# Kernel tuning notes

Measured on AMD Instinct MI355X. Metric: run time of the kernel, lower is better.

## Reference

```python
import jax, jax.numpy as jnp
import numpy as np
from jax import lax

B, C, H, W, K = 8, 128, 64, 64, 7
PAD = K // 2
TIMESTEPS = 8
BN_EPS = 1e-3


def _conv(x, w, pad):
    # x: [N,C,H,W], w: [O,I,kh,kw]
    return lax.conv_general_dilated(
        x, w, window_strides=(1, 1),
        padding=[(pad, pad), (pad, pad)],
        dimension_numbers=('NCHW', 'OIHW', 'NCHW'))


def _bn(x, g, b):
    # BatchNorm2d, track_running_stats=False -> always batch stats (biased var)
    m = jnp.mean(x, axis=(0, 2, 3), keepdims=True)
    v = jnp.var(x, axis=(0, 2, 3), keepdims=True)
    return (x - m) * lax.rsqrt(v + BN_EPS) * g[None, :, None, None] + b[None, :, None, None]


def _cb(b):
    return b[None, :, None, None]


def setup_inputs() -> dict:
    key = jax.random.key(0)
    ks = jax.random.split(key, 16)
    n = lambda k, sh, s=0.1: s * jax.random.normal(k, sh, dtype=jnp.float32)
    i_w_b = jax.random.uniform(ks[12], (C,), dtype=jnp.float32, minval=1.0, maxval=TIMESTEPS - 1.0)
    return {
        'input_': jax.random.normal(ks[0], (B, C, H, W), dtype=jnp.float32),
        'inhibition': jax.random.normal(ks[1], (B, C, H, W), dtype=jnp.float32),
        'excitation': jax.random.normal(ks[2], (B, C, H, W), dtype=jnp.float32),
        'a_w_w': n(ks[3], (1, C, K, K)), 'a_w_b': jnp.ones((1,), jnp.float32),
        'a_u_w': n(ks[4], (1, C, K, K)), 'a_u_b': jnp.ones((1,), jnp.float32),
        'i_w_w': n(ks[5], (C, C, 1, 1)), 'i_w_b': i_w_b,
        'i_u_w': n(ks[6], (C, C, 1, 1)), 'i_u_b': n(ks[7], (C,)),
        'e_w_w': n(ks[8], (C, C, 1, 1)), 'e_w_b': -i_w_b,
        'e_u_w': n(ks[9], (C, C, 1, 1)), 'e_u_b': n(ks[10], (C,)),
        'w_inh': n(ks[11], (C, C, K, K), 0.02),
        'w_exc': n(ks[13], (C, C, K, K), 0.02),
        'alpha': 0.1 * jnp.ones((C, 1, 1), jnp.float32),
        'gamma': jnp.ones((C, 1, 1), jnp.float32),
        'kappa': 0.5 * jnp.ones((C, 1, 1), jnp.float32),
        'w_param': 0.5 * jnp.ones((C, 1, 1), jnp.float32),
        'mu': jnp.ones((C, 1, 1), jnp.float32),
        'bn0_g': 0.1 * jnp.ones((C,), jnp.float32), 'bn0_b': jnp.zeros((C,), jnp.float32),
        'bn1_g': 0.1 * jnp.ones((C,), jnp.float32), 'bn1_b': jnp.zeros((C,), jnp.float32),
    }


def reference(input_, inhibition, excitation,
              a_w_w, a_w_b, a_u_w, a_u_b,
              i_w_w, i_w_b, i_u_w, i_u_b,
              e_w_w, e_w_b, e_u_w, e_u_b,
              w_inh, w_exc, alpha, gamma, kappa, w_param, mu,
              bn0_g, bn0_b, bn1_g, bn1_b):
    att_gate = jax.nn.sigmoid(_conv(input_, a_w_w, PAD) + _cb(a_w_b)
                              + _conv(excitation, a_u_w, PAD) + _cb(a_u_b))
    inh_intx = _bn(_conv(excitation * att_gate, w_inh, PAD), bn0_g, bn0_b)
    gated_inhibition = inhibition * att_gate
    gated_input = input_ * att_gate
    inhibition_hat = jnp.tanh(gated_input - jnp.tanh(inh_intx * (alpha * gated_inhibition + mu)))
    inh_gate = jax.nn.sigmoid(_conv(input_, i_w_w, 0) + _cb(i_w_b)
                              + _conv(inhibition, i_u_w, 0) + _cb(i_u_b))
    inhibition = (1.0 - inh_gate) * inhibition + inh_gate * inhibition_hat
    exc_gate = jax.nn.sigmoid(_conv(inhibition, e_w_w, 0) + _cb(e_w_b)
                              + _conv(excitation, e_u_w, 0) + _cb(e_u_b))
    exc_intx = _bn(_conv(inhibition, w_exc, PAD), bn1_g, bn1_b)
    excitation_hat = jnp.tanh(kappa * inhibition + gamma * exc_intx + w_param * inhibition * exc_intx)
    excitation = (1.0 - exc_gate) * excitation + exc_gate * excitation_hat
    return (inhibition, excitation)
```

## Files before the change

### kernel.cpp

```cpp
#include <hip/hip_runtime.h>
#include <cstddef>

typedef _Float16 f16;
typedef _Float16 f16x8 __attribute__((ext_vector_type(8)));
typedef float f32x16 __attribute__((ext_vector_type(16)));

#define Bc   8
#define Cc   128
#define Hc   64
#define Wc   64
#define HWc  4096
#define PADc 3
#define TAPS 49

#define PY 8
#define PX 16
#define WY 14
#define WX 22
#define NPOS (WY*WX)
#define AROW 256
#define ALDS_BYTES (NPOS*AROW)

__global__ __launch_bounds__(256) void prep_kernel(
    const float* __restrict__ w1, const float* __restrict__ w2,
    f16* __restrict__ wt1, f16* __restrict__ wt2, float* __restrict__ att)
{
    int idx = blockIdx.x*256 + threadIdx.x;
    const int NW = TAPS*Cc*Cc;
    if (idx < NW) {
        int tap = idx / (Cc*Cc);
        int rem = idx - tap*(Cc*Cc);
        int co = rem >> 7, ci = rem & 127;
        size_t src = (size_t)(co*Cc + ci)*TAPS + tap;
        wt1[idx] = (f16)w1[src];
        wt2[idx] = (f16)w2[src];
    }
    if (idx < Bc*HWc) att[idx] = 0.f;
}

__global__ __launch_bounds__(128) void att_partial(
    const float* __restrict__ input_, const float* __restrict__ exc,
    const float* __restrict__ aw, const float* __restrict__ au,
    float* __restrict__ att)
{
    __shared__ float wsa[32*49];
    __shared__ float wsb[32*49];
    __shared__ float ti[WY*WX];
    __shared__ float te[WY*WX];
    const int tid = threadIdx.x;
    const int tile = blockIdx.x;
    const int cch  = blockIdx.y*32;
    const int b    = blockIdx.z;
    for (int i = tid; i < 32*49; i += 128) { wsa[i] = aw[cch*49 + i]; wsb[i] = au[cch*49 + i]; }
    const int y0 = (tile >> 2)*8, x0 = (tile & 3)*16;
    const int tx = tid & 15, ty = tid >> 4;
    const float* ib = input_ + (size_t)b*Cc*HWc;
    const float* eb = exc    + (size_t)b*Cc*HWc;
    float acc = 0.f;
    for (int ci = 0; ci < 32; ++ci) {
        __syncthreads();
        for (int i = tid; i < WY*WX; i += 128) {
            int iy = i / WX, ix = i - iy*WX;
            int gy = y0 + iy - PADc, gx = x0 + ix - PADc;
            float v0 = 0.f, v1 = 0.f;
            if (gy >= 0 && gy < Hc && gx >= 0 && gx < Wc) {
                size_t o = (size_t)(cch+ci)*HWc + gy*Wc + gx;
                v0 = ib[o]; v1 = eb[o];
            }
            ti[i] = v0; te[i] = v1;
        }
        __syncthreads();
        const float* wa = &wsa[ci*49];
        const float* wb = &wsb[ci*49];
        #pragma unroll
        for (int kh = 0; kh < 7; ++kh) {
            #pragma unroll
            for (int kw = 0; kw < 7; ++kw) {
                const int k = kh*7+kw;
                acc += ti[(ty+kh)*WX + tx+kw] * wa[k];
                acc += te[(ty+kh)*WX + tx+kw] * wb[k];
            }
        }
    }
    atomicAdd(&att[(size_t)b*HWc + (size_t)(y0+ty)*Wc + (x0+tx)], acc);
}

__global__ __launch_bounds__(256) void att_final(
    float* __restrict__ att, const float* __restrict__ awb, const float* __restrict__ aub)
{
    int i = blockIdx.x*256 + threadIdx.x;
    float z = att[i] + awb[0] + aub[0];
    att[i] = 1.f/(1.f+expf(-z));
}

__global__ __launch_bounds__(256) void conv7_mfma(
    const float* __restrict__ x, const float* __restrict__ att,
    const f16* __restrict__ wt, float* __restrict__ out)
{
    __shared__ unsigned char smem[ALDS_BYTES];
    const int tid = threadIdx.x;
    const int x0 = blockIdx.x * PX;
    const int y0 = blockIdx.y * PY;
    const int b  = blockIdx.z;
    const float* xb = x + (size_t)b*Cc*HWc;

    for (int idx = tid; idx < NPOS*16; idx += 256) {
        int slot = idx / NPOS;
        int pos  = idx - slot*NPOS;
        int r = pos / WX, xw = pos - r*WX;
        int gy = y0 + r - PADc, gx = x0 + xw - PADc;
        bool inb = (gy >= 0 && gy < Hc && gx >= 0 && gx < Wc);
        float g = 1.f;
        if (att) g = inb ? att[(size_t)b*HWc + gy*Wc + gx] : 0.f;
        unsigned int pk[4];
        #pragma unroll
        for (int jj = 0; jj < 4; ++jj) {
            float v0 = 0.f, v1 = 0.f;
            if (inb) {
                size_t o = (size_t)(slot*8 + jj*2)*HWc + (size_t)gy*Wc + gx;
                v0 = xb[o]; v1 = xb[o + HWc];
            }
            f16 h0 = (f16)(v0*g), h1 = (f16)(v1*g);
            unsigned short u0 = __builtin_bit_cast(unsigned short, h0);
            unsigned short u1 = __builtin_bit_cast(unsigned short, h1);
            pk[jj] = (unsigned int)u0 | ((unsigned int)u1 << 16);
        }
        *(uint4*)(smem + pos*AROW + ((slot ^ (pos & 15)) << 4)) =
            make_uint4(pk[0], pk[1], pk[2], pk[3]);
    }
    __syncthreads();

    const int l   = tid & 63;
    const int wid = tid >> 6;
    const int wco = (wid >> 1) << 6;
    const int wpy = (wid & 1) << 2;
    const int lr  = l & 31;
    const int hi  = l >> 5;
    const int yA  = wpy + (lr >> 4);
    const int xA  = lr & 15;

    f32x16 acc00 = {}, acc01 = {}, acc10 = {}, acc11 = {};

    const f16* wrow0 = wt + (size_t)(wco      + lr)*Cc + hi*8;
    const f16* wrow1 = wt + (size_t)(wco + 32 + lr)*Cc + hi*8;

    for (int t = 0; t < TAPS; ++t) {
        const int kh = t / 7, kw = t - kh*7;
        const int pos0 = (yA + kh)*WX + xA + kw;
        const int pos1 = pos0 + 2*WX;
        const size_t tapoff = (size_t)t*Cc*Cc;
        #pragma unroll
        for (int s = 0; s < 8; ++s) {
            const int slot = (s << 1) + hi;
            f16x8 a0 = *(const f16x8*)(wrow0 + tapoff + s*16);
            f16x8 a1 = *(const f16x8*)(wrow1 + tapoff + s*16);
            f16x8 b0 = *(const f16x8*)(smem + pos0*AROW + ((slot ^ (pos0 & 15)) << 4));
            f16x8 b1 = *(const f16x8*)(smem + pos1*AROW + ((slot ^ (pos1 & 15)) << 4));
            acc00 = __builtin_amdgcn_mfma_f32_32x32x16_f16(a0, b0, acc00, 0, 0, 0);
            acc01 = __builtin_amdgcn_mfma_f32_32x32x16_f16(a0, b1, acc01, 0, 0, 0);
            acc10 = __builtin_amdgcn_mfma_f32_32x32x16_f16(a1, b0, acc10, 0, 0, 0);
            acc11 = __builtin_amdgcn_mfma_f32_32x32x16_f16(a1, b1, acc11, 0, 0, 0);
        }
    }

    const int xg = x0 + xA;
    #pragma unroll
    for (int r = 0; r < 16; ++r) {
        const int cr = (r & 3) + 8*(r >> 2) + 4*hi;
        const int y00 = y0 + wpy + 0 + (lr >> 4);
        const int y01 = y0 + wpy + 2 + (lr >> 4);
        out[((size_t)b*Cc + wco      + cr)*HWc + (size_t)y00*Wc + xg] = acc00[r];
        out[((size_t)b*Cc + wco      + cr)*HWc + (size_t)y01*Wc + xg] = acc01[r];
        out[((size_t)b*Cc + wco + 32 + cr)*HWc + (size_t)y00*Wc + xg] = acc10[r];
        out[((size_t)b*Cc + wco + 32 + cr)*HWc + (size_t)y01*Wc + xg] = acc11[r];
    }
}

__global__ __launch_bounds__(256) void bn_stats_kernel(
    const float* __restrict__ x, const float* __restrict__ g,
    const float* __restrict__ bta, float* __restrict__ sc, float* __restrict__ bi)
{
    const int c = blockIdx.x;
    const int tid = threadIdx.x;
    float s = 0.f, s2 = 0.f;
    for (int i = tid; i < Bc*HWc; i += 256) {
        int b = i >> 12;
        int p = i & (HWc-1);
        float v = x[((size_t)b*Cc + c)*HWc + p];
        s += v; s2 += v*v;
    }
    #pragma unroll
    for (int off = 32; off > 0; off >>= 1) {
        s  += __shfl_down(s,  off);
        s2 += __shfl_down(s2, off);
    }
    __shared__ float ls[4], ls2[4];
    const int wv = tid >> 6;
    if ((tid & 63) == 0) { ls[wv] = s; ls2[wv] = s2; }
    __syncthreads();
    if (tid == 0) {
        s  = ls[0]+ls[1]+ls[2]+ls[3];
        s2 = ls2[0]+ls2[1]+ls2[2]+ls2[3];
        const float n = (float)(Bc*HWc);
        float m   = s / n;
        float var = s2 / n - m*m;
        float r   = rsqrtf(var + 1e-3f);
        float scale = r * g[c];
        sc[c] = scale;
        bi[c] = bta[c] - m*scale;
    }
}

#define GCO 32

__global__ __launch_bounds__(256) void gate_i_kernel(
    const float* __restrict__ input_, const float* __restrict__ inh,
    const float* __restrict__ iw, const float* __restrict__ iwb,
    const float* __restrict__ uw, const float* __restrict__ uwb,
    const float* c1, const float* __restrict__ sc, const float* __restrict__ bi,
    const float* __restrict__ att,
    const float* __restrict__ alpha, const float* __restrict__ mu,
    float* out)
{
    __shared__ float swi[Cc][GCO];
    __shared__ float swu[Cc][GCO];
    const int tid = threadIdx.x;
    const int p0  = blockIdx.x * 256;
    const int cob = blockIdx.y * GCO;
    const int b   = blockIdx.z;
    for (int i = tid; i < Cc*GCO; i += 256) {
        int ci = i / GCO, co = i % GCO;
        swi[ci][co] = iw[(size_t)(cob+co)*Cc + ci];
        swu[ci][co] = uw[(size_t)(cob+co)*Cc + ci];
    }
    __syncthreads();
    const int p = p0 + tid;
    const float* xb = input_ + (size_t)b*Cc*HWc + p;
    const float* hb = inh    + (size_t)b*Cc*HWc + p;
    float acc[GCO];
    #pragma unroll
    for (int i = 0; i < GCO; ++i) acc[i] = 0.f;
    #pragma unroll 4
    for (int ci = 0; ci < Cc; ++ci) {
        float xi = xb[(size_t)ci*HWc];
        float xu = hb[(size_t)ci*HWc];
        #pragma unroll
        for (int co = 0; co < GCO; ++co)
            acc[co] += xi*swi[ci][co] + xu*swu[ci][co];
    }
    const float a = att[(size_t)b*HWc + p];
    #pragma unroll
    for (int co = 0; co < GCO; ++co) {
        const int c = cob + co;
        float hv = hb[(size_t)c*HWc];
        float g  = 1.f/(1.f+expf(-(acc[co] + iwb[c] + uwb[c])));
        size_t idx = ((size_t)b*Cc + c)*HWc + p;
        float intx = c1[idx]*sc[c] + bi[c];
        float gi = xb[(size_t)c*HWc] * a;
        float gh = hv * a;
        float ihat = tanhf(gi - tanhf(intx*(alpha[c]*gh + mu[c])));
        out[idx] = (1.f-g)*hv + g*ihat;
    }
}

__global__ __launch_bounds__(256) void gate_e_kernel(
    const float* __restrict__ inh_new, const float* __restrict__ exc,
    const float* __restrict__ ew, const float* __restrict__ ewb,
    const float* __restrict__ uw, const float* __restrict__ uwb,
    const float* c2, const float* __restrict__ sc, const float* __restrict__ bi,
    const float* __restrict__ kappa, const float* __restrict__ gamma_,
    const float* __restrict__ wp,
    float* out)
{
    __shared__ float swe[Cc][GCO];
    __shared__ float swu[Cc][GCO];
    const int tid = threadIdx.x;
    const int p0  = blockIdx.x * 256;
    const int cob = blockIdx.y * GCO;
    const int b   = blockIdx.z;
    for (int i = tid; i < Cc*GCO; i += 256) {
        int ci = i / GCO, co = i % GCO;
        swe[ci][co] = ew[(size_t)(cob+co)*Cc + ci];
        swu[ci][co] = uw[(size_t)(cob+co)*Cc + ci];
    }
    __syncthreads();
    const int p = p0 + tid;
    const float* hb = inh_new + (size_t)b*Cc*HWc + p;
    const float* eb = exc     + (size_t)b*Cc*HWc + p;
    float acc[GCO];
    #pragma unroll
    for (int i = 0; i < GCO; ++i) acc[i] = 0.f;
    #pragma unroll 4
    for (int ci = 0; ci < Cc; ++ci) {
        float xi = hb[(size_t)ci*HWc];
        float xu = eb[(size_t)ci*HWc];
        #pragma unroll
        for (int co = 0; co < GCO; ++co)
            acc[co] += xi*swe[ci][co] + xu*swu[ci][co];
    }
    #pragma unroll
    for (int co = 0; co < GCO; ++co) {
        const int c = cob + co;
        float hv = hb[(size_t)c*HWc];
        float ev = eb[(size_t)c*HWc];
        float g  = 1.f/(1.f+expf(-(acc[co] + ewb[c] + uwb[c])));
        size_t idx = ((size_t)b*Cc + c)*HWc + p;
        float intx = c2[idx]*sc[c] + bi[c];
        float ehat = tanhf(kappa[c]*hv + gamma_[c]*intx + wp[c]*hv*intx);
        out[idx] = (1.f-g)*ev + g*ehat;
    }
}

extern "C" void kernel_launch(void* const* d_in, const int* in_sizes, int n_in,
                              void* d_out, int out_size, void* d_ws, size_t ws_size,
                              hipStream_t stream)
{
    (void)in_sizes; (void)n_in; (void)out_size; (void)ws_size;
    const float* input_ = (const float*)d_in[0];
    const float* inh    = (const float*)d_in[1];
    const float* exc    = (const float*)d_in[2];
    const float* a_w_w  = (const float*)d_in[3];
    const float* a_w_b  = (const float*)d_in[4];
    const float* a_u_w  = (const float*)d_in[5];
    const float* a_u_b  = (const float*)d_in[6];
    const float* i_w_w  = (const float*)d_in[7];
    const float* i_w_b  = (const float*)d_in[8];
    const float* i_u_w  = (const float*)d_in[9];
    const float* i_u_b  = (const float*)d_in[10];
    const float* e_w_w  = (const float*)d_in[11];
    const float* e_w_b  = (const float*)d_in[12];
    const float* e_u_w  = (const float*)d_in[13];
    const float* e_u_b  = (const float*)d_in[14];
    const float* w_inh  = (const float*)d_in[15];
    const float* w_exc  = (const float*)d_in[16];
    const float* alpha  = (const float*)d_in[17];
    const float* gamma_ = (const float*)d_in[18];
    const float* kappa  = (const float*)d_in[19];
    const float* w_par  = (const float*)d_in[20];
    const float* mu     = (const float*)d_in[21];
    const float* bn0_g  = (const float*)d_in[22];
    const float* bn0_b  = (const float*)d_in[23];
    const float* bn1_g  = (const float*)d_in[24];
    const float* bn1_b  = (const float*)d_in[25];

    float* out = (float*)d_out;
    const size_t N = (size_t)Bc*Cc*HWc;
    float* c1 = out;
    float* c2 = out + N;

    float* att = (float*)d_ws;
    float* sc0 = att + 32768;
    float* bi0 = sc0 + Cc;
    float* sc1 = bi0 + Cc;
    float* bi1 = sc1 + Cc;
    f16* wt1 = (f16*)((char*)d_ws + 33280u*4u);
    f16* wt2 = wt1 + (size_t)TAPS*Cc*Cc;

    prep_kernel<<<(TAPS*Cc*Cc + 255)/256, 256, 0, stream>>>(w_inh, w_exc, wt1, wt2, att);
    att_partial<<<dim3(32, 4, Bc), 128, 0, stream>>>(input_, exc, a_w_w, a_u_w, att);
    att_final<<<(Bc*HWc)/256, 256, 0, stream>>>(att, a_w_b, a_u_b);
    conv7_mfma<<<dim3(4, 8, Bc), 256, 0, stream>>>(exc, att, wt1, c1);
    bn_stats_kernel<<<Cc, 256, 0, stream>>>(c1, bn0_g, bn0_b, sc0, bi0);
    gate_i_kernel<<<dim3(HWc/256, Cc/GCO, Bc), 256, 0, stream>>>(
        input_, inh, i_w_w, i_w_b, i_u_w, i_u_b, c1, sc0, bi0, att, alpha, mu, out);
    conv7_mfma<<<dim3(4, 8, Bc), 256, 0, stream>>>(out, nullptr, wt2, c2);
    bn_stats_kernel<<<Cc, 256, 0, stream>>>(c2, bn1_g, bn1_b, sc1, bi1);
    gate_e_kernel<<<dim3(HWc/256, Cc/GCO, Bc), 256, 0, stream>>>(
        out, exc, e_w_w, e_w_b, e_u_w, e_u_b, c2, sc1, bi1, kappa, gamma_, w_par, out + N);
}
```

Baseline: 786.6 us.

## Compute 1x1 gate convolutions with fp16 MFMA instead of scalar fp32 loops

The inhibition and excitation gate kernels now stage both input tensors for a 128-pixel tile into swizzled LDS as fp16. They compute the concatenated 256-wide 1x1 convolution with 32x32x16 MFMA, using fp16 weights packed in the prep kernel, and then apply the fused gating epilogue. This removes the scalar FMA loop and the repeated input reads across output-channel blocks. The cost is fp16 rounding in the gate pre-activations and fewer, larger blocks with 64KB of LDS each.

```diff
diff --git a/kernel.cpp b/kernel.cpp
--- a/kernel.cpp
+++ b/kernel.cpp
@@ -23,7 +23,11 @@
 
 __global__ __launch_bounds__(256) void prep_kernel(
     const float* __restrict__ w1, const float* __restrict__ w2,
-    f16* __restrict__ wt1, f16* __restrict__ wt2, float* __restrict__ att)
+    const float* __restrict__ iww, const float* __restrict__ iuw,
+    const float* __restrict__ eww, const float* __restrict__ euw,
+    f16* __restrict__ wt1, f16* __restrict__ wt2,
+    f16* __restrict__ wgi, f16* __restrict__ wge,
+    float* __restrict__ att)
 {
     int idx = blockIdx.x*256 + threadIdx.x;
     const int NW = TAPS*Cc*Cc;
@@ -34,6 +38,11 @@
         size_t src = (size_t)(co*Cc + ci)*TAPS + tap;
         wt1[idx] = (f16)w1[src];
         wt2[idx] = (f16)w2[src];
+    }
+    if (idx < 2*Cc*Cc) {
+        int co = idx >> 8, k = idx & 255;
+        wgi[idx] = (f16)((k < 128) ? iww[co*Cc + k] : iuw[co*Cc + (k-128)]);
+        wge[idx] = (f16)((k < 128) ? eww[co*Cc + k] : euw[co*Cc + (k-128)]);
     }
     if (idx < Bc*HWc) att[idx] = 0.f;
 }
@@ -137,7 +146,7 @@
     const int lr  = l & 31;
     const int hi  = l >> 5;
     const int yA  = wpy + (lr >> 4);
-    const int xA  = lr & 15;
+    const int xA  = l & 15;
 
     f32x16 acc00 = {}, acc01 = {}, acc10 = {}, acc11 = {};
 
@@ -211,103 +220,192 @@
     }
 }
 
-#define GCO 32
-
-__global__ __launch_bounds__(256) void gate_i_kernel(
+__global__ __launch_bounds__(256) void gate_i_mfma(
     const float* __restrict__ input_, const float* __restrict__ inh,
-    const float* __restrict__ iw, const float* __restrict__ iwb,
-    const float* __restrict__ uw, const float* __restrict__ uwb,
+    const f16* __restrict__ wg,
+    const float* __restrict__ iwb, const float* __restrict__ uwb,
     const float* c1, const float* __restrict__ sc, const float* __restrict__ bi,
     const float* __restrict__ att,
     const float* __restrict__ alpha, const float* __restrict__ mu,
     float* out)
 {
-    __shared__ float swi[Cc][GCO];
-    __shared__ float swu[Cc][GCO];
+    __shared__ unsigned char bsm[128*512];
+    __shared__ float sbias[Cc], ssc[Cc], sbi[Cc], sal[Cc], smu[Cc];
     const int tid = threadIdx.x;
-    const int p0  = blockIdx.x * 256;
-    const int cob = blockIdx.y * GCO;
-    const int b   = blockIdx.z;
-    for (int i = tid; i < Cc*GCO; i += 256) {
-        int ci = i / GCO, co = i % GCO;
-        swi[ci][co] = iw[(size_t)(cob+co)*Cc + ci];
-        swu[ci][co] = uw[(size_t)(cob+co)*Cc + ci];
+    const int p0 = blockIdx.x * 128;
+    const int b  = blockIdx.y;
+    if (tid < Cc) {
+        sbias[tid] = iwb[tid] + uwb[tid];
+        ssc[tid] = sc[tid]; sbi[tid] = bi[tid];
+        sal[tid] = alpha[tid]; smu[tid] = mu[tid];
+    }
+    const float* xb = input_ + (size_t)b*Cc*HWc + p0;
+    const float* hb = inh    + (size_t)b*Cc*HWc + p0;
+    #pragma unroll
+    for (int it = 0; it < 16; ++it) {
+        int idx = tid + it*256;
+        int px = idx & 127, slot = idx >> 7;
+        const float* src = (slot < 16) ? (xb + (size_t)(slot*8)*HWc)
+                                       : (hb + (size_t)((slot-16)*8)*HWc);
+        unsigned int pk[4];
+        #pragma unroll
+        for (int jj = 0; jj < 4; ++jj) {
+            f16 h0 = (f16)src[(size_t)(jj*2  )*HWc + px];
+            f16 h1 = (f16)src[(size_t)(jj*2+1)*HWc + px];
+            pk[jj] = (unsigned)__builtin_bit_cast(unsigned short, h0)
+                   | ((unsigned)__builtin_bit_cast(unsigned short, h1) << 16);
+        }
+        *(uint4*)(bsm + px*512 + ((slot ^ (px & 31)) << 4)) =
+            make_uint4(pk[0], pk[1], pk[2], pk[3]);
     }
     __syncthreads();
-    const int p = p0 + tid;
-    const float* xb = input_ + (size_t)b*Cc*HWc + p;
-    const float* hb = inh    + (size_t)b*Cc*HWc + p;
-    float acc[GCO];
-    #pragma unroll
-    for (int i = 0; i < GCO; ++i) acc[i] = 0.f;
-    #pragma unroll 4
-    for (int ci = 0; ci < Cc; ++ci) {
-        float xi = xb[(size_t)ci*HWc];
-        float xu = hb[(size_t)ci*HWc];
-        #pragma unroll
-        for (int co = 0; co < GCO; ++co)
-            acc[co] += xi*swi[ci][co] + xu*swu[ci][co];
-    }
-    const float a = att[(size_t)b*HWc + p];
-    #pragma unroll
-    for (int co = 0; co < GCO; ++co) {
-        const int c = cob + co;
-        float hv = hb[(size_t)c*HWc];
-        float g  = 1.f/(1.f+expf(-(acc[co] + iwb[c] + uwb[c])));
-        size_t idx = ((size_t)b*Cc + c)*HWc + p;
-        float intx = c1[idx]*sc[c] + bi[c];
-        float gi = xb[(size_t)c*HWc] * a;
-        float gh = hv * a;
-        float ihat = tanhf(gi - tanhf(intx*(alpha[c]*gh + mu[c])));
-        out[idx] = (1.f-g)*hv + g*ihat;
-    }
-}
-
-__global__ __launch_bounds__(256) void gate_e_kernel(
-    const float* __restrict__ inh_new, const float* __restrict__ exc,
-    const float* __restrict__ ew, const float* __restrict__ ewb,
-    const float* __restrict__ uw, const float* __restrict__ uwb,
+
+    const int l   = tid & 63;
+    const int wid = tid >> 6;
+    const int wco = (wid >> 1) << 6;
+    const int wpx = (wid & 1) << 6;
+    const int lr  = l & 31;
+    const int hi  = l >> 5;
+
+    f32x16 acc00 = {}, acc01 = {}, acc10 = {}, acc11 = {};
+    const f16* wr0 = wg + (size_t)(wco      + lr)*256 + hi*8;
+    const f16* wr1 = wg + (size_t)(wco + 32 + lr)*256 + hi*8;
+    const unsigned char* br0 = bsm + (size_t)(wpx      + lr)*512;
+    const unsigned char* br1 = bsm + (size_t)(wpx + 32 + lr)*512;
+    #pragma unroll
+    for (int s = 0; s < 16; ++s) {
+        const int slot = 2*s + hi;
+        const int swz = (slot ^ lr) << 4;
+        f16x8 a0 = *(const f16x8*)(wr0 + s*16);
+        f16x8 a1 = *(const f16x8*)(wr1 + s*16);
+        f16x8 b0 = *(const f16x8*)(br0 + swz);
+        f16x8 b1 = *(const f16x8*)(br1 + swz);
+        acc00 = __builtin_amdgcn_mfma_f32_32x32x16_f16(a0, b0, acc00, 0, 0, 0);
+        acc01 = __builtin_amdgcn_mfma_f32_32x32x16_f16(a0, b1, acc01, 0, 0, 0);
+        acc10 = __builtin_amdgcn_mfma_f32_32x32x16_f16(a1, b0, acc10, 0, 0, 0);
+        acc11 = __builtin_amdgcn_mfma_f32_32x32x16_f16(a1, b1, acc11, 0, 0, 0);
+    }
+
+    const int pA = p0 + wpx + lr;
+    const int pB = pA + 32;
+    const float aA = att[(size_t)b*HWc + pA];
+    const float aB = att[(size_t)b*HWc + pB];
+    #pragma unroll
+    for (int r = 0; r < 16; ++r) {
+        const int cr = (r & 3) + 8*(r >> 2) + 4*hi;
+        const int c0 = wco + cr, c1i = wco + 32 + cr;
+        const float bz0 = sbias[c0], bz1 = sbias[c1i];
+        const float sc0v = ssc[c0], sc1v = ssc[c1i];
+        const float bi0v = sbi[c0], bi1v = sbi[c1i];
+        const float al0 = sal[c0], al1 = sal[c1i];
+        const float mu0 = smu[c0], mu1 = smu[c1i];
+        #pragma unroll
+        for (int q = 0; q < 4; ++q) {
+            const int cc = (q < 2) ? c0 : c1i;
+            const int pp = (q & 1) ? pB : pA;
+            const float av = (q & 1) ? aB : aA;
+            const float z = (q==0)?acc00[r]:(q==1)?acc01[r]:(q==2)?acc10[r]:acc11[r];
+            const float bz = (q < 2) ? bz0 : bz1;
+            const float scv = (q < 2) ? sc0v : sc1v;
+            const float biv = (q < 2) ? bi0v : bi1v;
+            const float alv = (q < 2) ? al0 : al1;
+            const float muv = (q < 2) ? mu0 : mu1;
+            size_t idx = ((size_t)b*Cc + cc)*HWc + pp;
+            float hv = inh[idx];
+            float xi = input_[idx];
+            float intx = c1[idx]*scv + biv;
+            float g = 1.f/(1.f+expf(-(z + bz)));
+            float ihat = tanhf(xi*av - tanhf(intx*(alv*(hv*av) + muv)));
+            out[idx] = (1.f-g)*hv + g*ihat;
+        }
+    }
+}
+
+__global__ __launch_bounds__(256) void gate_e_mfma(
+    const float* __restrict__ hnew, const float* __restrict__ exc,
+    const f16* __restrict__ wg,
+    const float* __restrict__ ewb, const float* __restrict__ uwb,
     const float* c2, const float* __restrict__ sc, const float* __restrict__ bi,
     const float* __restrict__ kappa, const float* __restrict__ gamma_,
     const float* __restrict__ wp,
     float* out)
 {
-    __shared__ float swe[Cc][GCO];
-    __shared__ float swu[Cc][GCO];
+    __shared__ unsigned char bsm[128*512];
+    __shared__ float sbias[Cc], ssc[Cc], sbi[Cc], skp[Cc], sgm[Cc], swp[Cc];
     const int tid = threadIdx.x;
-    const int p0  = blockIdx.x * 256;
-    const int cob = blockIdx.y * GCO;
-    const int b   = blockIdx.z;
-    for (int i = tid; i < Cc*GCO; i += 256) {
-        int ci = i / GCO, co = i % GCO;
-        swe[ci][co] = ew[(size_t)(cob+co)*Cc + ci];
-        swu[ci][co] = uw[(size_t)(cob+co)*Cc + ci];
+    const int p0 = blockIdx.x * 128;
+    const int b  = blockIdx.y;
+    if (tid < Cc) {
+        sbias[tid] = ewb[tid] + uwb[tid];
+        ssc[tid] = sc[tid]; sbi[tid] = bi[tid];
+        skp[tid] = kappa[tid]; sgm[tid] = gamma_[tid]; swp[tid] = wp[tid];
+    }
+    const float* xb = hnew + (size_t)b*Cc*HWc + p0;
+    const float* eb = exc  + (size_t)b*Cc*HWc + p0;
+    #pragma unroll
+    for (int it = 0; it < 16; ++it) {
+        int idx = tid + it*256;
+        int px = idx & 127, slot = idx >> 7;
+        const float* src = (slot < 16) ? (xb + (size_t)(slot*8)*HWc)
+                                       : (eb + (size_t)((slot-16)*8)*HWc);
+        unsigned int pk[4];
+        #pragma unroll
+        for (int jj = 0; jj < 4; ++jj) {
+            f16 h0 = (f16)src[(size_t)(jj*2  )*HWc + px];
+            f16 h1 = (f16)src[(size_t)(jj*2+1)*HWc + px];
+            pk[jj] = (unsigned)__builtin_bit_cast(unsigned short, h0)
+                   | ((unsigned)__builtin_bit_cast(unsigned short, h1) << 16);
+        }
+        *(uint4*)(bsm + px*512 + ((slot ^ (px & 31)) << 4)) =
+            make_uint4(pk[0], pk[1], pk[2], pk[3]);
     }
     __syncthreads();
-    const int p = p0 + tid;
-    const float* hb = inh_new + (size_t)b*Cc*HWc + p;
-    const float* eb = exc     + (size_t)b*Cc*HWc + p;
-    float acc[GCO];
-    #pragma unroll
-    for (int i = 0; i < GCO; ++i) acc[i] = 0.f;
-    #pragma unroll 4
-    for (int ci = 0; ci < Cc; ++ci) {
-        float xi = hb[(size_t)ci*HWc];
-        float xu = eb[(size_t)ci*HWc];
-        #pragma unroll
-        for (int co = 0; co < GCO; ++co)
-            acc[co] += xi*swe[ci][co] + xu*swu[ci][co];
-    }
-    #pragma unroll
-    for (int co = 0; co < GCO; ++co) {
-        const int c = cob + co;
-        float hv = hb[(size_t)c*HWc];
-        float ev = eb[(size_t)c*HWc];
-        float g  = 1.f/(1.f+expf(-(acc[co] + ewb[c] + uwb[c])));
-        size_t idx = ((size_t)b*Cc + c)*HWc + p;
-        float intx = c2[idx]*sc[c] + bi[c];
-        float ehat = tanhf(kappa[c]*hv + gamma_[c]*intx + wp[c]*hv*intx);
-        out[idx] = (1.f-g)*ev + g*ehat;
+
+    const int l   = tid & 63;
+    const int wid = tid >> 6;
+    const int wco = (wid >> 1) << 6;
+    const int wpx = (wid & 1) << 6;
+    const int lr  = l & 31;
+    const int hi  = l >> 5;
+
+    f32x16 acc00 = {}, acc01 = {}, acc10 = {}, acc11 = {};
+    const f16* wr0 = wg + (size_t)(wco      + lr)*256 + hi*8;
+    const f16* wr1 = wg + (size_t)(wco + 32 + lr)*256 + hi*8;
+    const unsigned char* br0 = bsm + (size_t)(wpx      + lr)*512;
+    const unsigned char* br1 = bsm + (size_t)(wpx + 32 + lr)*512;
+    #pragma unroll
+    for (int s = 0; s < 16; ++s) {
+        const int slot = 2*s + hi;
+        const int swz = (slot ^ lr) << 4;
+        f16x8 a0 = *(const f16x8*)(wr0 + s*16);
+        f16x8 a1 = *(const f16x8*)(wr1 + s*16);
+        f16x8 b0 = *(const f16x8*)(br0 + swz);
+        f16x8 b1 = *(const f16x8*)(br1 + swz);
+        acc00 = __builtin_amdgcn_mfma_f32_32x32x16_f16(a0, b0, acc00, 0, 0, 0);
+        acc01 = __builtin_amdgcn_mfma_f32_32x32x16_f16(a0, b1, acc01, 0, 0, 0);
+        acc10 = __builtin_amdgcn_mfma_f32_32x32x16_f16(a1, b0, acc10, 0, 0, 0);
+        acc11 = __builtin_amdgcn_mfma_f32_32x32x16_f16(a1, b1, acc11, 0, 0, 0);
+    }
+
+    const int pA = p0 + wpx + lr;
+    const int pB = pA + 32;
+    #pragma unroll
+    for (int r = 0; r < 16; ++r) {
+        const int cr = (r & 3) + 8*(r >> 2) + 4*hi;
+        const int c0 = wco + cr, c1i = wco + 32 + cr;
+        #pragma unroll
+        for (int q = 0; q < 4; ++q) {
+            const int cc = (q < 2) ? c0 : c1i;
+            const int pp = (q & 1) ? pB : pA;
+            const float z = (q==0)?acc00[r]:(q==1)?acc01[r]:(q==2)?acc10[r]:acc11[r];
+            size_t idx = ((size_t)b*Cc + cc)*HWc + pp;
+            float hv = hnew[idx];
+            float ev = exc[idx];
+            float intx = c2[idx]*ssc[cc] + sbi[cc];
+            float g = 1.f/(1.f+expf(-(z + sbias[cc])));
+            float ehat = tanhf(skp[cc]*hv + sgm[cc]*intx + swp[cc]*hv*intx);
+            out[idx] = (1.f-g)*ev + g*ehat;
+        }
     }
 }
 
@@ -355,16 +453,19 @@
     float* bi1 = sc1 + Cc;
     f16* wt1 = (f16*)((char*)d_ws + 33280u*4u);
     f16* wt2 = wt1 + (size_t)TAPS*Cc*Cc;
-
-    prep_kernel<<<(TAPS*Cc*Cc + 255)/256, 256, 0, stream>>>(w_inh, w_exc, wt1, wt2, att);
+    f16* wgi = wt2 + (size_t)TAPS*Cc*Cc;
+    f16* wge = wgi + 2*Cc*Cc;
+
+    prep_kernel<<<(TAPS*Cc*Cc + 255)/256, 256, 0, stream>>>(
+        w_inh, w_exc, i_w_w, i_u_w, e_w_w, e_u_w, wt1, wt2, wgi, wge, att);
     att_partial<<<dim3(32, 4, Bc), 128, 0, stream>>>(input_, exc, a_w_w, a_u_w, att);
     att_final<<<(Bc*HWc)/256, 256, 0, stream>>>(att, a_w_b, a_u_b);
     conv7_mfma<<<dim3(4, 8, Bc), 256, 0, stream>>>(exc, att, wt1, c1);
     bn_stats_kernel<<<Cc, 256, 0, stream>>>(c1, bn0_g, bn0_b, sc0, bi0);
-    gate_i_kernel<<<dim3(HWc/256, Cc/GCO, Bc), 256, 0, stream>>>(
-        input_, inh, i_w_w, i_w_b, i_u_w, i_u_b, c1, sc0, bi0, att, alpha, mu, out);
+    gate_i_mfma<<<dim3(HWc/128, Bc), 256, 0, stream>>>(
+        input_, inh, wgi, i_w_b, i_u_b, c1, sc0, bi0, att, alpha, mu, out);
     conv7_mfma<<<dim3(4, 8, Bc), 256, 0, stream>>>(out, nullptr, wt2, c2);
     bn_stats_kernel<<<Cc, 256, 0, stream>>>(c2, bn1_g, bn1_b, sc1, bi1);
-    gate_e_kernel<<<dim3(HWc/256, Cc/GCO, Bc), 256, 0, stream>>>(
-        out, exc, e_w_w, e_w_b, e_u_w, e_u_b, c2, sc1, bi1, kappa, gamma_, w_par, out + N);
-}
+    gate_e_mfma<<<dim3(HWc/128, Bc), 256, 0, stream>>>(
+        out, exc, wge, e_w_b, e_u_b, c2, sc1, bi1, kappa, gamma_, w_par, out + N);
+}
```

Measured after the change: 640.8 us. 1.23x faster.
